# Optimization experiments

Measured on AMD Instinct MI355X. Metric: run time of the kernel, lower is better.

The kernel has to match this reference:

```python
import jax, jax.numpy as jnp
import numpy as np

VOXEL_SIZE = np.array([0.2, 0.2, 4.0], dtype=np.float32)
PC_MIN = np.array([0.0, -40.0, -3.0], dtype=np.float32)
BN_EPS = 1e-3
N_POINTS = 1_500_000
N_VOXELS = 200_000
C_IN = 7   # (4 - 3) + 6 stats channels (cluster offset + voxel-center offset)
C_OUT = 64


def setup_inputs() -> dict:
    key = jax.random.key(0)
    ks = jax.random.split(key, 8)
    features = jax.random.normal(ks[0], (N_POINTS, 4), dtype=jnp.float32)
    point2voxel = jax.random.randint(ks[1], (N_POINTS,), 0, N_VOXELS).astype(jnp.int32)
    voxel_coors = jnp.stack([
        jax.random.randint(ks[2], (N_VOXELS,), 0, 2),    # batch idx
        jnp.zeros((N_VOXELS,), jnp.int32),               # z (pillars -> 0)
        jax.random.randint(ks[3], (N_VOXELS,), 0, 400),  # y bin
        jax.random.randint(ks[4], (N_VOXELS,), 0, 352),  # x bin
    ], axis=1).astype(jnp.int32)
    W = jax.random.normal(ks[5], (C_IN, C_OUT), dtype=jnp.float32) * 0.1
    bn_gamma = jnp.ones((C_OUT,), jnp.float32)
    bn_beta = jnp.zeros((C_OUT,), jnp.float32)
    bn_mean = jax.random.normal(ks[6], (C_OUT,), dtype=jnp.float32) * 0.01
    bn_var = jax.random.uniform(ks[7], (C_OUT,), minval=0.5, maxval=1.5, dtype=jnp.float32)
    return dict(features=features, W=W, bn_gamma=bn_gamma, bn_beta=bn_beta,
                bn_mean=bn_mean, bn_var=bn_var, point2voxel=point2voxel,
                voxel_coors=voxel_coors)


def reference(features, W, bn_gamma, bn_beta, bn_mean, bn_var, point2voxel, voxel_coors):
    M = voxel_coors.shape[0]
    xyz = features[:, :3]

    # --- stats: cluster-center offset (per-voxel mean of xyz, mapped back) ---
    cnt = jax.ops.segment_sum(jnp.ones((xyz.shape[0],), xyz.dtype), point2voxel,
                              num_segments=M)
    vmean = jax.ops.segment_sum(xyz, point2voxel, num_segments=M)
    vmean = vmean / jnp.maximum(cnt, 1.0)[:, None]
    cluster_off = xyz - vmean[point2voxel]

    # --- stats: voxel-center offset ---
    vs = jnp.asarray(VOXEL_SIZE)
    mn = jnp.asarray(PC_MIN)
    # coors layout is (batch, z, y, x) -> take (x, y, z)
    centers = (voxel_coors[:, jnp.array([3, 2, 1])].astype(jnp.float32) + 0.5) * vs + mn
    center_off = xyz - centers[point2voxel]

    feats = jnp.concatenate([cluster_off, center_off, features[:, 3:]], axis=-1)  # [N,7]

    # --- PFN layer: Linear(bias=False) + BN1d (eval stats) + ReLU ---
    h = feats @ W
    h = (h - bn_mean) * jax.lax.rsqrt(bn_var + BN_EPS) * bn_gamma + bn_beta
    h = jax.nn.relu(h)

    # --- scatter max-reduce to voxels ---
    vfeats = jax.ops.segment_max(h, point2voxel, num_segments=M)
    vfeats = jnp.where(jnp.isfinite(vfeats), vfeats, 0.0)  # guard rare empty voxels
    return vfeats, voxel_coors
```

## Files before the change

kernel.cpp:

```cpp
#include <hip/hip_runtime.h>


#define BBITS 6
#define BVOX  (1 << BBITS)
#define PCAP  768
#define NR    (PCAP / 256)
#define NBLK  64
#define BMAX  3200

__global__ __launch_bounds__(256) void hist_k(const int* __restrict__ p2v,
                                              int* __restrict__ mat,
                                              int N, int NB, int chunk) {
    __shared__ int h[BMAX];
    int b = blockIdx.x, tid = threadIdx.x;
    for (int k = tid; k < NB; k += 256) h[k] = 0;
    __syncthreads();
    int s = b * chunk, e = min(N, s + chunk);
    for (int i = s + tid; i < e; i += 256)
        atomicAdd(&h[p2v[i] >> BBITS], 1);
    __syncthreads();
    for (int k = tid; k < NB; k += 256) mat[k * NBLK + b] = h[k];
}

__global__ void scanA_k(int* __restrict__ a, int* __restrict__ bsum, int S) {
    __shared__ int s[256];
    int tid = threadIdx.x;
    int base = blockIdx.x * 1024 + tid * 4;
    int c0 = (base + 0 < S) ? a[base + 0] : 0;
    int c1 = (base + 1 < S) ? a[base + 1] : 0;
    int c2 = (base + 2 < S) ? a[base + 2] : 0;
    int c3 = (base + 3 < S) ? a[base + 3] : 0;
    int tsum = c0 + c1 + c2 + c3;
    s[tid] = tsum;
    __syncthreads();
    for (int off = 1; off < 256; off <<= 1) {
        int v = (tid >= off) ? s[tid - off] : 0;
        __syncthreads();
        s[tid] += v;
        __syncthreads();
    }
    int excl = s[tid] - tsum;
    if (base + 0 < S) a[base + 0] = excl;
    if (base + 1 < S) a[base + 1] = excl + c0;
    if (base + 2 < S) a[base + 2] = excl + c0 + c1;
    if (base + 3 < S) a[base + 3] = excl + c0 + c1 + c2;
    if (tid == 255) bsum[blockIdx.x] = s[255];
}

__global__ void scanB_k(int* __restrict__ bsum, int nb) {
    __shared__ int s[256];
    int tid = threadIdx.x;
    int v = (tid < nb) ? bsum[tid] : 0;
    s[tid] = v;
    __syncthreads();
    for (int off = 1; off < 256; off <<= 1) {
        int t = (tid >= off) ? s[tid - off] : 0;
        __syncthreads();
        s[tid] += t;
        __syncthreads();
    }
    if (tid < nb) bsum[tid] = s[tid] - v;
}

__global__ void scanC_k(int* __restrict__ a, const int* __restrict__ bsum, int S) {
    int i = blockIdx.x * blockDim.x + threadIdx.x;
    if (i < S) a[i] += bsum[i >> 10];
}

__global__ __launch_bounds__(256) void scatter_kidx_k(const int* __restrict__ p2v,
                                                      const int* __restrict__ mat,
                                                      int* __restrict__ keyidx,
                                                      int N, int NB, int chunk) {
    __shared__ int cur[BMAX];
    int b = blockIdx.x, tid = threadIdx.x;
    for (int k = tid; k < NB; k += 256) cur[k] = mat[k * NBLK + b];
    __syncthreads();
    int s = b * chunk, e = min(N, s + chunk);
    for (int i = s + tid; i < e; i += 256) {
        int v = p2v[i];
        int k = v >> BBITS;
        int pos = atomicAdd(&cur[k], 1);
        keyidx[pos] = (i << BBITS) | (v & (BVOX - 1));
    }
}

__global__ __launch_bounds__(256, 4) void gather_bucket_k(
    const float4* __restrict__ feats, const int* __restrict__ keyidx,
    const int* __restrict__ mat, const float* __restrict__ W,
    const float* __restrict__ gamma, const float* __restrict__ beta,
    const float* __restrict__ mean, const float* __restrict__ var,
    const int* __restrict__ coors,
    float* __restrict__ out_v, float* __restrict__ out_c,
    int M, int NB, int N) {
    __shared__ float4 s_pay[PCAP];
    __shared__ int    s_cnt[BVOX];
    __shared__ int    s_off[BVOX];
    __shared__ int    s_cur[BVOX];
    __shared__ float4 s_cen[BVOX];

    int bk = blockIdx.x, tid = threadIdx.x;
    int lane = tid & 63, w = tid >> 6;

    float w0 = W[0 * 64 + lane], w1 = W[1 * 64 + lane], w2 = W[2 * 64 + lane];
    float w3 = W[3 * 64 + lane], w4 = W[4 * 64 + lane], w5 = W[5 * 64 + lane];
    float w6 = W[6 * 64 + lane];
    float u0 = w0 + w3, u1 = w1 + w4, u2 = w2 + w5, u3 = w6;
    float sc = gamma[lane] * rsqrtf(var[lane] + 1e-3f);
    float bi = beta[lane] - mean[lane] * sc;
    bool take_max = (sc >= 0.0f);

    int s = mat[bk * NBLK];
    int e = (bk + 1 < NB) ? mat[(bk + 1) * NBLK] : N;
    int L = min(e - s, PCAP);

    int pk[NR];
    float4 fv[NR];
#pragma unroll
    for (int r = 0; r < NR; ++r) {
        int j = tid + r * 256;
        pk[r] = (j < L) ? keyidx[s + j] : -1;
    }
#pragma unroll
    for (int r = 0; r < NR; ++r)
        if (pk[r] >= 0) fv[r] = feats[pk[r] >> BBITS];

    if (tid < BVOX) s_cnt[tid] = 0;
    __syncthreads();
#pragma unroll
    for (int r = 0; r < NR; ++r)
        if (pk[r] >= 0) atomicAdd(&s_cnt[pk[r] & (BVOX - 1)], 1);

    int vbase = bk << BBITS;
    if (tid < BVOX) {
        int vg = vbase + tid;
        if (vg < M) {
            int4 cc = ((const int4*)coors)[vg];
            ((float4*)out_c)[vg] = make_float4((float)cc.x, (float)cc.y,
                                               (float)cc.z, (float)cc.w);
            s_cen[tid] = make_float4((cc.w + 0.5f) * 0.2f,
                                     (cc.z + 0.5f) * 0.2f - 40.0f,
                                     (cc.y + 0.5f) * 4.0f - 3.0f, 0.0f);
        }
    }
    __syncthreads();

    if (w == 0) {
        int c = s_cnt[lane];
        int x = c;
        for (int off = 1; off < 64; off <<= 1) {
            int t = __shfl_up(x, off);
            if (lane >= off) x += t;
        }
        int ex = x - c;
        s_off[lane] = ex;
        s_cur[lane] = ex;
    }
    __syncthreads();

#pragma unroll
    for (int r = 0; r < NR; ++r)
        if (pk[r] >= 0) {
            int vox = pk[r] & (BVOX - 1);
            int pos = atomicAdd(&s_cur[vox], 1);
            s_pay[pos] = fv[r];
        }
    __syncthreads();

    int lv0 = w << 4;
    int cnts[16];
#pragma unroll
    for (int q = 0; q < 16; ++q) cnts[q] = s_cnt[lv0 + q];
    int st = s_off[lv0];

    for (int q = 0; q < 16; ++q) {
        int lv = lv0 + q;
        int v = vbase + lv;
        int npts = cnts[q];
        float4 cen = s_cen[lv];
        float sx = 0.f, sy = 0.f, sz = 0.f;
        float amax = -3.402823466e+38f, amin = 3.402823466e+38f;
        int i = 0;
        for (; i + 3 < npts; i += 4) {
            float4 f0 = s_pay[st + i + 0];
            float4 f1 = s_pay[st + i + 1];
            float4 f2 = s_pay[st + i + 2];
            float4 f3 = s_pay[st + i + 3];
            sx += f0.x + f1.x + f2.x + f3.x;
            sy += f0.y + f1.y + f2.y + f3.y;
            sz += f0.z + f1.z + f2.z + f3.z;
            float a0 = f0.x * u0 + f0.y * u1 + f0.z * u2 + f0.w * u3;
            float a1 = f1.x * u0 + f1.y * u1 + f1.z * u2 + f1.w * u3;
            float a2 = f2.x * u0 + f2.y * u1 + f2.z * u2 + f2.w * u3;
            float a3 = f3.x * u0 + f3.y * u1 + f3.z * u2 + f3.w * u3;
            amax = fmaxf(fmaxf(fmaxf(amax, a0), fmaxf(a1, a2)), a3);
            amin = fminf(fminf(fminf(amin, a0), fminf(a1, a2)), a3);
        }
        for (; i < npts; ++i) {
            float4 f = s_pay[st + i];
            sx += f.x; sy += f.y; sz += f.z;
            float a = f.x * u0 + f.y * u1 + f.z * u2 + f.w * u3;
            amax = fmaxf(amax, a);
            amin = fminf(amin, a);
        }
        float res = 0.0f;
        if (npts > 0) {
            float inv = 1.0f / (float)npts;
            float mx = sx * inv, my = sy * inv, mz = sz * inv;
            float K = mx * w0 + my * w1 + mz * w2 +
                      cen.x * w3 + cen.y * w4 + cen.z * w5;
            float aext = take_max ? amax : amin;
            res = fmaxf((aext - K) * sc + bi, 0.0f);
        }
        if (v < M) out_v[(size_t)v * 64 + lane] = res;
        st += npts;
    }
}

extern "C" void kernel_launch(void* const* d_in, const int* in_sizes, int n_in,
                              void* d_out, int out_size, void* d_ws, size_t ws_size,
                              hipStream_t stream) {
    const float* features = (const float*)d_in[0];
    const float* W        = (const float*)d_in[1];
    const float* gamma    = (const float*)d_in[2];
    const float* beta     = (const float*)d_in[3];
    const float* mean     = (const float*)d_in[4];
    const float* var      = (const float*)d_in[5];
    const int*   p2v      = (const int*)d_in[6];
    const int*   coors    = (const int*)d_in[7];
    int N = in_sizes[0] / 4;
    int M = in_sizes[7] / 4;

    int NB = (M + BVOX - 1) >> BBITS;
    int S = NB * NBLK;
    int chunk = (N + NBLK - 1) / NBLK;

    int* mat    = (int*)d_ws;
    int* bsum   = mat + S;
    int* keyidx = bsum + 256;

    float* out_v = (float*)d_out;
    float* out_c = out_v + (size_t)M * 64;

    hist_k<<<NBLK, 256, 0, stream>>>(p2v, mat, N, NB, chunk);
    int nbA = (S + 1023) / 1024;
    scanA_k<<<nbA, 256, 0, stream>>>(mat, bsum, S);
    scanB_k<<<1, 256, 0, stream>>>(bsum, nbA);
    scanC_k<<<(S + 255) / 256, 256, 0, stream>>>(mat, bsum, S);
    scatter_kidx_k<<<NBLK, 256, 0, stream>>>(p2v, mat, keyidx, N, NB, chunk);
    gather_bucket_k<<<NB, 256, 0, stream>>>(
        (const float4*)features, keyidx, mat, W, gamma, beta, mean, var,
        coors, out_v, out_c, M, NB, N);
}
```

Baseline: 145.2 us.

## Use more histogram blocks, widen scan tiles, sign-fold min/max, raise occupancy

Raises the number of point-chunk blocks for the histogram and scatter passes from 64 to 256, giving more parallelism across the device. The scan now handles 16 elements per thread (4096 per block) so the larger count matrix still fits in one second-level scan. In the gather kernel the weights are pre-multiplied by the sign of the BN scale, so only a running max is tracked instead of both max and min. The launch-bound occupancy hint is also raised from 4 to 8. The cost is a count matrix four times larger to scan and scatter, and possible register pressure from the higher occupancy hint.

```diff
diff --git a/kernel.cpp b/kernel.cpp
--- a/kernel.cpp
+++ b/kernel.cpp
@@ -5,8 +5,9 @@
 #define BVOX  (1 << BBITS)
 #define PCAP  768
 #define NR    (PCAP / 256)
-#define NBLK  64
+#define NBLK  256
 #define BMAX  3200
+#define SCH   4096
 
 __global__ __launch_bounds__(256) void hist_k(const int* __restrict__ p2v,
                                               int* __restrict__ mat,
@@ -25,12 +26,14 @@
 __global__ void scanA_k(int* __restrict__ a, int* __restrict__ bsum, int S) {
     __shared__ int s[256];
     int tid = threadIdx.x;
-    int base = blockIdx.x * 1024 + tid * 4;
-    int c0 = (base + 0 < S) ? a[base + 0] : 0;
-    int c1 = (base + 1 < S) ? a[base + 1] : 0;
-    int c2 = (base + 2 < S) ? a[base + 2] : 0;
-    int c3 = (base + 3 < S) ? a[base + 3] : 0;
-    int tsum = c0 + c1 + c2 + c3;
+    int base = blockIdx.x * SCH + tid * 16;
+    int c[16];
+    int tsum = 0;
+#pragma unroll
+    for (int j = 0; j < 16; ++j) {
+        c[j] = (base + j < S) ? a[base + j] : 0;
+        tsum += c[j];
+    }
     s[tid] = tsum;
     __syncthreads();
     for (int off = 1; off < 256; off <<= 1) {
@@ -39,11 +42,12 @@
         s[tid] += v;
         __syncthreads();
     }
-    int excl = s[tid] - tsum;
-    if (base + 0 < S) a[base + 0] = excl;
-    if (base + 1 < S) a[base + 1] = excl + c0;
-    if (base + 2 < S) a[base + 2] = excl + c0 + c1;
-    if (base + 3 < S) a[base + 3] = excl + c0 + c1 + c2;
+    int run = s[tid] - tsum;
+#pragma unroll
+    for (int j = 0; j < 16; ++j) {
+        if (base + j < S) a[base + j] = run;
+        run += c[j];
+    }
     if (tid == 255) bsum[blockIdx.x] = s[255];
 }
 
@@ -64,7 +68,7 @@
 
 __global__ void scanC_k(int* __restrict__ a, const int* __restrict__ bsum, int S) {
     int i = blockIdx.x * blockDim.x + threadIdx.x;
-    if (i < S) a[i] += bsum[i >> 10];
+    if (i < S) a[i] += bsum[i / SCH];
 }
 
 __global__ __launch_bounds__(256) void scatter_kidx_k(const int* __restrict__ p2v,
@@ -84,7 +88,7 @@
     }
 }
 
-__global__ __launch_bounds__(256, 4) void gather_bucket_k(
+__global__ __launch_bounds__(256, 8) void gather_bucket_k(
     const float4* __restrict__ feats, const int* __restrict__ keyidx,
     const int* __restrict__ mat, const float* __restrict__ W,
     const float* __restrict__ gamma, const float* __restrict__ beta,
@@ -104,10 +108,11 @@
     float w0 = W[0 * 64 + lane], w1 = W[1 * 64 + lane], w2 = W[2 * 64 + lane];
     float w3 = W[3 * 64 + lane], w4 = W[4 * 64 + lane], w5 = W[5 * 64 + lane];
     float w6 = W[6 * 64 + lane];
-    float u0 = w0 + w3, u1 = w1 + w4, u2 = w2 + w5, u3 = w6;
     float sc = gamma[lane] * rsqrtf(var[lane] + 1e-3f);
     float bi = beta[lane] - mean[lane] * sc;
-    bool take_max = (sc >= 0.0f);
+    float sgn = (sc >= 0.0f) ? 1.0f : -1.0f;
+    float u0 = sgn * (w0 + w3), u1 = sgn * (w1 + w4);
+    float u2 = sgn * (w2 + w5), u3 = sgn * w6;
 
     int s = mat[bk * NBLK];
     int e = (bk + 1 < NB) ? mat[(bk + 1) * NBLK] : N;
@@ -178,7 +183,7 @@
         int npts = cnts[q];
         float4 cen = s_cen[lv];
         float sx = 0.f, sy = 0.f, sz = 0.f;
-        float amax = -3.402823466e+38f, amin = 3.402823466e+38f;
+        float amax = -3.402823466e+38f;
         int i = 0;
         for (; i + 3 < npts; i += 4) {
             float4 f0 = s_pay[st + i + 0];
@@ -193,14 +198,12 @@
             float a2 = f2.x * u0 + f2.y * u1 + f2.z * u2 + f2.w * u3;
             float a3 = f3.x * u0 + f3.y * u1 + f3.z * u2 + f3.w * u3;
             amax = fmaxf(fmaxf(fmaxf(amax, a0), fmaxf(a1, a2)), a3);
-            amin = fminf(fminf(fminf(amin, a0), fminf(a1, a2)), a3);
         }
         for (; i < npts; ++i) {
             float4 f = s_pay[st + i];
             sx += f.x; sy += f.y; sz += f.z;
             float a = f.x * u0 + f.y * u1 + f.z * u2 + f.w * u3;
             amax = fmaxf(amax, a);
-            amin = fminf(amin, a);
         }
         float res = 0.0f;
         if (npts > 0) {
@@ -208,7 +211,7 @@
             float mx = sx * inv, my = sy * inv, mz = sz * inv;
             float K = mx * w0 + my * w1 + mz * w2 +
                       cen.x * w3 + cen.y * w4 + cen.z * w5;
-            float aext = take_max ? amax : amin;
+            float aext = sgn * amax;
             res = fmaxf((aext - K) * sc + bi, 0.0f);
         }
         if (v < M) out_v[(size_t)v * 64 + lane] = res;
@@ -242,7 +245,7 @@
     float* out_c = out_v + (size_t)M * 64;
 
     hist_k<<<NBLK, 256, 0, stream>>>(p2v, mat, N, NB, chunk);
-    int nbA = (S + 1023) / 1024;
+    int nbA = (S + SCH - 1) / SCH;
     scanA_k<<<nbA, 256, 0, stream>>>(mat, bsum, S);
     scanB_k<<<1, 256, 0, stream>>>(bsum, nbA);
     scanC_k<<<(S + 255) / 256, 256, 0, stream>>>(mat, bsum, S);
```

Result: faster. 135.5 us (-6.7%).
